# Kernel optimization log

Hardware: AMD Instinct MI355X
Metric: run time of the kernel (lower is better)

## Reference

```python
import jax, jax.numpy as jnp
import numpy as np

N = 100000   # nodes
E = 1600000  # edges
F = 128      # feature / hidden dim
G = 512      # graphs in batch
L = 3        # conv layers
EPS = 1e-5   # batchnorm eps


def _gcn_conv(h, W, b, src, dst, dinv):
    # GCNConv: out = D^{-1/2} (A + I) D^{-1/2} (h W) + b
    hw = h @ W                                   # [N, F]
    norm = dinv[src] * dinv[dst]                 # [E]
    agg = jax.ops.segment_sum(hw[src] * norm[:, None], dst, num_segments=N)
    agg = agg + hw * (dinv * dinv)[:, None]      # self-loop contribution
    return agg + b


def _batchnorm(h, gamma, beta):
    # training-mode BN: batch statistics over the node dimension
    mu = h.mean(axis=0)
    var = h.var(axis=0)
    return gamma * (h - mu) * jax.lax.rsqrt(var + EPS) + beta


def setup_inputs() -> dict:
    key = jax.random.key(0)
    ks = jax.random.split(key, 8)
    x = jax.random.normal(ks[0], (N, F), dtype=jnp.float32)
    edge_index = jax.random.randint(ks[1], (2, E), 0, N)
    batch = jnp.sort(jax.random.randint(ks[2], (N,), 0, G))
    Ws = jax.random.normal(ks[3], (L, F, F), dtype=jnp.float32) / np.float32(np.sqrt(F))
    bs = jnp.zeros((L, F), jnp.float32)
    gammas = jnp.ones((L, F), jnp.float32)
    betas = jnp.zeros((L, F), jnp.float32)
    H = 64  # max(hidden//2, 16)
    w1 = jax.random.normal(ks[4], (2 * F, H), dtype=jnp.float32) / np.float32(np.sqrt(2 * F))
    b1 = jnp.zeros((H,), jnp.float32)
    w2 = jax.random.normal(ks[5], (H, 1), dtype=jnp.float32) / np.float32(np.sqrt(H))
    b2 = jnp.zeros((1,), jnp.float32)
    return dict(x=x, edge_index=edge_index, batch=batch, Ws=Ws, bs=bs,
                gammas=gammas, betas=betas, w1=w1, b1=b1, w2=w2, b2=b2)


def reference(x, edge_index, batch, Ws, bs, gammas, betas, w1, b1, w2, b2):
    src, dst = edge_index[0], edge_index[1]
    # symmetric gcn_norm degrees (self-loops included)
    deg = jax.ops.segment_sum(jnp.ones((E,), x.dtype), dst, num_segments=N) + 1.0
    dinv = jax.lax.rsqrt(deg)
    h = x
    for i in range(L):
        h = _gcn_conv(h, Ws[i], bs[i], src, dst, dinv)
        h = _batchnorm(h, gammas[i], betas[i])
        h = jax.nn.relu(h)  # dropout inactive (eval)
    counts = jax.ops.segment_sum(jnp.ones((N,), h.dtype), batch, num_segments=G)
    mean_pool = jax.ops.segment_sum(h, batch, num_segments=G) / jnp.maximum(counts, 1.0)[:, None]
    max_pool = jax.ops.segment_max(h, batch, num_segments=G)
    max_pool = jnp.where(jnp.isfinite(max_pool), max_pool, 0.0)  # empty segments -> 0
    z = jnp.concatenate([mean_pool, max_pool], axis=1)  # [G, 2F]
    z = jax.nn.relu(z @ w1 + b1)
    return z @ w2 + b2  # [G, 1]
```

## Files before the change

kernel.cpp:

```cpp
#include <hip/hip_runtime.h>
#include <hip/hip_fp16.h>


constexpr int F = 128;
constexpr float BN_EPS = 1e-5f;
constexpr int NB1 = 256;
constexpr int NBKT = 256;

typedef _Float16 f16x8 __attribute__((ext_vector_type(8)));
typedef float f32x4 __attribute__((ext_vector_type(4)));

__global__ void hist_k(const int* __restrict__ dst, int* __restrict__ degi, int E) {
  int stride = gridDim.x * blockDim.x;
  for (int e = blockIdx.x * blockDim.x + threadIdx.x; e < E; e += stride)
    atomicAdd(&degi[dst[e]], 1);
}

__global__ __launch_bounds__(256) void scanA_k(const int* __restrict__ degi, int* __restrict__ bsums,
                                               float* __restrict__ dinv, int n) {
  __shared__ int red[256];
  int tid = threadIdx.x;
  int base = blockIdx.x * 1024 + tid * 4;
  int4 v = *(const int4*)(degi + base);
  if (base + 0 < n) dinv[base + 0] = rsqrtf((float)v.x + 1.0f);
  if (base + 1 < n) dinv[base + 1] = rsqrtf((float)v.y + 1.0f);
  if (base + 2 < n) dinv[base + 2] = rsqrtf((float)v.z + 1.0f);
  if (base + 3 < n) dinv[base + 3] = rsqrtf((float)v.w + 1.0f);
  red[tid] = v.x + v.y + v.z + v.w;
  __syncthreads();
  for (int off = 128; off > 0; off >>= 1) {
    if (tid < off) red[tid] += red[tid + off];
    __syncthreads();
  }
  if (tid == 0) bsums[blockIdx.x] = red[0];
}

__global__ void scanB_k(int* __restrict__ bsums, int nb, int* __restrict__ rowptr, int N) {
  __shared__ int sh[1024];
  int tid = threadIdx.x;
  for (int i = tid; i < nb; i += blockDim.x) sh[i] = bsums[i];
  __syncthreads();
  if (tid == 0) {
    int run = 0;
    for (int i = 0; i < nb; ++i) { int t = sh[i]; sh[i] = run; run += t; }
    rowptr[N] = run;
  }
  __syncthreads();
  for (int i = tid; i < nb; i += blockDim.x) bsums[i] = sh[i];
}

__global__ __launch_bounds__(256) void scanC_k(const int* __restrict__ degi, const int* __restrict__ bsums,
                                               int* __restrict__ rowptr, int n) {
  __shared__ int ts[256];
  int tid = threadIdx.x;
  int base = blockIdx.x * 1024 + tid * 4;
  int4 v = *(const int4*)(degi + base);
  int e0 = v.x, e1 = v.y, e2 = v.z, e3 = v.w;
  int tot = e0 + e1 + e2 + e3;
  ts[tid] = tot;
  __syncthreads();
  for (int off = 1; off < 256; off <<= 1) {
    int add = (tid >= off) ? ts[tid - off] : 0;
    __syncthreads();
    ts[tid] += add;
    __syncthreads();
  }
  int excl = ts[tid] - tot + bsums[blockIdx.x];
  int p0 = excl, p1 = p0 + e0, p2 = p1 + e1, p3 = p2 + e2;
  if (base + 0 < n) rowptr[base + 0] = p0;
  if (base + 1 < n) rowptr[base + 1] = p1;
  if (base + 2 < n) rowptr[base + 2] = p2;
  if (base + 3 < n) rowptr[base + 3] = p3;
}

__global__ __launch_bounds__(256) void part1_k(const int* __restrict__ dst, int* __restrict__ hist, int E) {
  __shared__ int cnt[NBKT];
  int tid = threadIdx.x;
  cnt[tid] = 0;
  __syncthreads();
  int chunk = (E + NB1 - 1) / NB1;
  int s = blockIdx.x * chunk, e = min(s + chunk, E);
  for (int i = s + tid; i < e; i += 256) atomicAdd(&cnt[dst[i] >> 9], 1);
  __syncthreads();
  hist[blockIdx.x * NBKT + tid] = cnt[tid];
}

__global__ __launch_bounds__(1024) void part_scan_k(const int* __restrict__ hist, int* __restrict__ base) {
  __shared__ int sh[1024];
  const int t = threadIdx.x;
  const int per = (NBKT * NB1) / 1024;
  int sum = 0;
  for (int j = 0; j < per; ++j) {
    int i = t * per + j;
    sum += hist[(i & (NB1 - 1)) * NBKT + (i >> 8)];
  }
  sh[t] = sum;
  __syncthreads();
  for (int off = 1; off < 1024; off <<= 1) {
    int v = (t >= off) ? sh[t - off] : 0;
    __syncthreads();
    sh[t] += v;
    __syncthreads();
  }
  int run = sh[t] - sum;
  for (int j = 0; j < per; ++j) {
    int i = t * per + j;
    int v = hist[(i & (NB1 - 1)) * NBKT + (i >> 8)];
    base[i] = run;
    run += v;
  }
}

__global__ __launch_bounds__(256) void part2_k(const int* __restrict__ src, const int* __restrict__ dst,
                                               const int* __restrict__ base, int2* __restrict__ pairbuf, int E) {
  __shared__ int cnt[NBKT];
  __shared__ int baseL[NBKT];
  int tid = threadIdx.x;
  cnt[tid] = 0;
  baseL[tid] = base[tid * NB1 + blockIdx.x];
  __syncthreads();
  int chunk = (E + NB1 - 1) / NB1;
  int s = blockIdx.x * chunk, e = min(s + chunk, E);
  for (int i = s + tid; i < e; i += 256) {
    int sv = src[i], dv = dst[i];
    int b = dv >> 9;
    int r = atomicAdd(&cnt[b], 1);
    pairbuf[baseL[b] + r] = make_int2(sv, dv);
  }
}

__global__ __launch_bounds__(256) void scat2_k(const int2* __restrict__ pairbuf, const int* __restrict__ base,
                                               const int* __restrict__ rowptr, int* __restrict__ cols,
                                               int N, int E) {
  __shared__ int curL[512];
  const int b = blockIdx.x;
  const int tid = threadIdx.x;
  const int n0 = b << 9;
  for (int i = tid; i < 512; i += 256) {
    int node = n0 + i;
    curL[i] = (node < N) ? rowptr[node] : 0;
  }
  __syncthreads();
  int lo = base[b * NB1];
  int hi = (b == NBKT - 1) ? E : base[(b + 1) * NB1];
  for (int t = lo + tid; t < hi; t += 256) {
    int2 pr = pairbuf[t];
    int pos = atomicAdd(&curL[pr.y - n0], 1);
    cols[pos] = pr.x;
  }
}

__global__ __launch_bounds__(128) void wprep_k(const float* __restrict__ W, __half* __restrict__ Wt) {
  const int b = blockIdx.x;
  const int k = threadIdx.x;
  const int l = b >> 7, c = b & 127;
  Wt[(size_t)b * 128 + k] = __float2half(W[(size_t)l * 16384 + k * 128 + c]);
}

__global__ void bnprep_k(const float* __restrict__ stats, const float* __restrict__ gamma,
                         const float* __restrict__ beta, float* __restrict__ scsh,
                         int first, float inv_n) {
  int c = threadIdx.x;
  if (first) { scsh[c] = 1.f; scsh[128 + c] = 0.f; return; }
  float mu = stats[c] * inv_n;
  float var = stats[128 + c] * inv_n - mu * mu;
  float sc = gamma[c] * rsqrtf(var + BN_EPS);
  scsh[c] = sc;
  scsh[128 + c] = beta[c] - mu * sc;
}

__global__ __launch_bounds__(256) void gemm_mfma_k(
    const float* __restrict__ A, const __half* __restrict__ Wt,
    __half* __restrict__ Ch, const float* __restrict__ scsh,
    const float* __restrict__ dinv, int n, int dorelu) {
  __shared__ char Al[64 * 256];
  const int tid = threadIdx.x;
  const int r0 = blockIdx.x * 64;

  {
    const int row = tid & 63;
    const int cb = tid >> 6;
    const int r = r0 + row;
    const int c0 = cb * 32;
    float4 va[8];
    if (r < n) {
      const float* ap = A + (size_t)r * F + c0;
#pragma unroll
      for (int j = 0; j < 8; ++j) va[j] = *(const float4*)(ap + j * 4);
    } else {
#pragma unroll
      for (int j = 0; j < 8; ++j) va[j] = make_float4(0.f, 0.f, 0.f, 0.f);
    }
    union { __half2 h2[16]; int4 q[4]; } u;
#pragma unroll
    for (int j = 0; j < 8; ++j) {
      float4 sc = *(const float4*)(scsh + c0 + j * 4);
      float4 sh = *(const float4*)(scsh + 128 + c0 + j * 4);
      float x0 = fmaf(va[j].x, sc.x, sh.x);
      float x1 = fmaf(va[j].y, sc.y, sh.y);
      float x2 = fmaf(va[j].z, sc.z, sh.z);
      float x3 = fmaf(va[j].w, sc.w, sh.w);
      if (dorelu) {
        x0 = fmaxf(x0, 0.f); x1 = fmaxf(x1, 0.f);
        x2 = fmaxf(x2, 0.f); x3 = fmaxf(x3, 0.f);
      }
      u.h2[2 * j]     = __floats2half2_rn(x0, x1);
      u.h2[2 * j + 1] = __floats2half2_rn(x2, x3);
    }
    const int rowb = row * 256;
    const int swz = (row & 7) << 4;
#pragma unroll
    for (int j = 0; j < 4; ++j) {
      int off = (rowb + cb * 64 + j * 16) ^ swz;
      *(int4*)(Al + off) = u.q[j];
    }
  }
  __syncthreads();

  const int w = tid >> 6, l = tid & 63;
  const int arow = w * 16 + (l & 15);
  const int kg = l >> 4;
  f16x8 af[4];
  {
    const int swz = (arow & 7) << 4;
    const int base = arow * 256 + kg * 16;
#pragma unroll
    for (int kc = 0; kc < 4; ++kc)
      af[kc] = *(const f16x8*)(Al + ((base + kc * 64) ^ swz));
  }
  const int orow = r0 + w * 16 + kg * 4;
  float4 dvv = *(const float4*)(dinv + orow);
  float dvr[4] = {dvv.x, dvv.y, dvv.z, dvv.w};

#pragma unroll
  for (int t = 0; t < 8; ++t) {
    const __half* wp = Wt + ((size_t)(t * 16 + (l & 15)) * 128 + kg * 8);
    f32x4 acc = {0.f, 0.f, 0.f, 0.f};
#pragma unroll
    for (int kc = 0; kc < 4; ++kc) {
      f16x8 bf = *(const f16x8*)(wp + kc * 32);
      acc = __builtin_amdgcn_mfma_f32_16x16x32_f16(af[kc], bf, acc, 0, 0, 0);
    }
    const int ccol = t * 16 + (l & 15);
#pragma unroll
    for (int rr = 0; rr < 4; ++rr) {
      int r = orow + rr;
      if (r < n) Ch[(size_t)r * F + ccol] = __float2half(acc[rr] * dvr[rr]);
    }
  }
}

__global__ __launch_bounds__(256) void spmm_k(const __half* __restrict__ hw, const int* __restrict__ rowptr,
                                              const int* __restrict__ cols, const float* __restrict__ dinv,
                                              const float* __restrict__ bias, float* __restrict__ out, int n) {
  int wid = (blockIdx.x * 256 + threadIdx.x) >> 6;
  int lane = threadIdx.x & 63;
  if (wid >= n) return;
  const __half2* hw2 = (const __half2*)hw;
  float2 vf = __half22float2(hw2[(size_t)wid * 64 + lane]);
  float ax = vf.x, ay = vf.y;
  int j = rowptr[wid];
  const int e = rowptr[wid + 1];
  for (; j + 8 <= e; j += 8) {
    int c0 = cols[j + 0], c1 = cols[j + 1], c2 = cols[j + 2], c3 = cols[j + 3];
    int c4 = cols[j + 4], c5 = cols[j + 5], c6 = cols[j + 6], c7 = cols[j + 7];
    float2 v0 = __half22float2(hw2[(size_t)c0 * 64 + lane]);
    float2 v1 = __half22float2(hw2[(size_t)c1 * 64 + lane]);
    float2 v2 = __half22float2(hw2[(size_t)c2 * 64 + lane]);
    float2 v3 = __half22float2(hw2[(size_t)c3 * 64 + lane]);
    float2 v4 = __half22float2(hw2[(size_t)c4 * 64 + lane]);
    float2 v5 = __half22float2(hw2[(size_t)c5 * 64 + lane]);
    float2 v6 = __half22float2(hw2[(size_t)c6 * 64 + lane]);
    float2 v7 = __half22float2(hw2[(size_t)c7 * 64 + lane]);
    ax += ((v0.x + v1.x) + (v2.x + v3.x)) + ((v4.x + v5.x) + (v6.x + v7.x));
    ay += ((v0.y + v1.y) + (v2.y + v3.y)) + ((v4.y + v5.y) + (v6.y + v7.y));
  }
  if (j + 4 <= e) {
    int c0 = cols[j + 0], c1 = cols[j + 1], c2 = cols[j + 2], c3 = cols[j + 3];
    float2 v0 = __half22float2(hw2[(size_t)c0 * 64 + lane]);
    float2 v1 = __half22float2(hw2[(size_t)c1 * 64 + lane]);
    float2 v2 = __half22float2(hw2[(size_t)c2 * 64 + lane]);
    float2 v3 = __half22float2(hw2[(size_t)c3 * 64 + lane]);
    ax += (v0.x + v1.x) + (v2.x + v3.x);
    ay += (v0.y + v1.y) + (v2.y + v3.y);
    j += 4;
  }
  for (; j < e; ++j) {
    float2 vv = __half22float2(hw2[(size_t)cols[j] * 64 + lane]);
    ax += vv.x;
    ay += vv.y;
  }
  float di = dinv[wid];
  float2 b = ((const float2*)bias)[lane];
  float2 o;
  o.x = fmaf(di, ax, b.x);
  o.y = fmaf(di, ay, b.y);
  ((float2*)out)[(size_t)wid * 64 + lane] = o;
}

__global__ __launch_bounds__(256) void stats_k(const float* __restrict__ h, float* __restrict__ stats, int n) {
  __shared__ float s1[256], s2[256];
  int tid = threadIdx.x;
  int c = tid & 127, half = tid >> 7;
  float a = 0.f, b = 0.f;
  for (int r = blockIdx.x * 2 + half; r < n; r += gridDim.x * 2) {
    float v = h[(size_t)r * F + c];
    a += v;
    b += v * v;
  }
  s1[tid] = a; s2[tid] = b;
  __syncthreads();
  if (tid < 128) {
    atomicAdd(&stats[c], s1[tid] + s1[tid + 128]);
    atomicAdd(&stats[F + c], s2[tid] + s2[tid + 128]);
  }
}

__global__ __launch_bounds__(256) void pool_mlp_k(
    const float* __restrict__ h, const int* __restrict__ batch,
    const float* __restrict__ stats, const float* __restrict__ gamma,
    const float* __restrict__ beta, const float* __restrict__ w1,
    const float* __restrict__ b1, const float* __restrict__ w2,
    const float* __restrict__ b2, float* __restrict__ out,
    int n, float inv_n) {
  __shared__ float psum[4][128];
  __shared__ float pmax[4][128];
  __shared__ float zsh[256];
  __shared__ float part[4][64];
  const int g = blockIdx.x;
  const int tid = threadIdx.x;
  const int wave = tid >> 6, lane = tid & 63;

  int lo = 0, hi = n;
  while (lo < hi) { int m = (lo + hi) >> 1; if (batch[m] < g) lo = m + 1; else hi = m; }
  const int s = lo;
  hi = n;
  while (lo < hi) { int m = (lo + hi) >> 1; if (batch[m] < g + 1) lo = m + 1; else hi = m; }
  const int e = lo;

  const int c = lane * 2;
  float2 st = *(const float2*)(stats + c);
  float2 sq = *(const float2*)(stats + F + c);
  float2 ga = *(const float2*)(gamma + c);
  float2 be = *(const float2*)(beta + c);
  float mu0 = st.x * inv_n, mu1 = st.y * inv_n;
  float sc0 = ga.x * rsqrtf(sq.x * inv_n - mu0 * mu0 + BN_EPS);
  float sc1 = ga.y * rsqrtf(sq.y * inv_n - mu1 * mu1 + BN_EPS);
  float sh0 = be.x - mu0 * sc0;
  float sh1 = be.y - mu1 * sc1;

  float sum0 = 0.f, sum1 = 0.f, mx0 = 0.f, mx1 = 0.f;
#pragma unroll 2
  for (int r = s + wave; r < e; r += 4) {
    float2 v = *(const float2*)(h + (size_t)r * F + c);
    float h0 = fmaxf(fmaf(v.x, sc0, sh0), 0.f);
    float h1 = fmaxf(fmaf(v.y, sc1, sh1), 0.f);
    sum0 += h0; sum1 += h1;
    mx0 = fmaxf(mx0, h0); mx1 = fmaxf(mx1, h1);
  }
  psum[wave][c] = sum0; psum[wave][c + 1] = sum1;
  pmax[wave][c] = mx0;  pmax[wave][c + 1] = mx1;
  __syncthreads();

  if (tid < 128) {
    float sm = psum[0][tid] + psum[1][tid] + psum[2][tid] + psum[3][tid];
    float mx = fmaxf(fmaxf(pmax[0][tid], pmax[1][tid]), fmaxf(pmax[2][tid], pmax[3][tid]));
    float ic = (e > s) ? 1.0f / (float)(e - s) : 0.f;
    zsh[tid] = sm * ic;
    zsh[128 + tid] = mx;
  }
  __syncthreads();

  {
    const int j = lane, q = wave;
    float acc = 0.f;
    const float* wq = w1 + (size_t)q * 64 * 64 + j;
#pragma unroll 8
    for (int i = 0; i < 64; ++i) acc = fmaf(zsh[q * 64 + i], wq[(size_t)i * 64], acc);
    part[q][j] = acc;
  }
  __syncthreads();

  if (tid < 64) {
    float hid = part[0][tid] + part[1][tid] + part[2][tid] + part[3][tid] + b1[tid];
    hid = fmaxf(hid, 0.f) * w2[tid];
    for (int off = 32; off > 0; off >>= 1) hid += __shfl_down(hid, off);
    if (tid == 0) out[g] = hid + b2[0];
  }
}

extern "C" void kernel_launch(void* const* d_in, const int* in_sizes, int n_in,
                              void* d_out, int out_size, void* d_ws, size_t ws_size,
                              hipStream_t stream) {
  const float* x      = (const float*)d_in[0];
  const int*   ei     = (const int*)d_in[1];
  const int*   batch  = (const int*)d_in[2];
  const float* Ws     = (const float*)d_in[3];
  const float* bsv    = (const float*)d_in[4];
  const float* gammas = (const float*)d_in[5];
  const float* betas  = (const float*)d_in[6];
  const float* w1     = (const float*)d_in[7];
  const float* b1     = (const float*)d_in[8];
  const float* w2     = (const float*)d_in[9];
  const float* b2     = (const float*)d_in[10];
  float* out = (float*)d_out;

  const int N = in_sizes[0] / F;
  const int E = in_sizes[1] / 2;
  const int G = out_size;
  const int L = in_sizes[3] / (F * F);
  const int* srcp = ei;
  const int* dstp = ei + E;
  const int NB = (N + 1023) / 1024;

  char* p = (char*)d_ws;
  auto carve = [&](size_t bytes) {
    char* r = p;
    p += (bytes + 255) & ~(size_t)255;
    return r;
  };
  int*    degi    = (int*)carve((size_t)NB * 1024 * 4);
  float*  dinv    = (float*)carve((size_t)N * 4);
  int*    rowptr  = (int*)carve(((size_t)N + 1) * 4);
  int*    colsb   = (int*)carve((size_t)E * 4);
  int*    bsums   = (int*)carve(4096);
  int*    hist    = (int*)carve((size_t)NB1 * NBKT * 4);
  int*    pbase   = (int*)carve((size_t)NB1 * NBKT * 4);
  int2*   pairbuf = (int2*)carve((size_t)E * 8);
  float*  bnstats = (float*)carve(2 * F * 4);
  float*  scsh    = (float*)carve(2 * F * 4);
  __half* wth     = (__half*)carve((size_t)L * F * F * 2);
  __half* hwh     = (__half*)carve((size_t)N * F * 2);
  float*  bufA    = (float*)carve((size_t)N * F * 4);
  (void)ws_size; (void)n_in;

  hipMemsetAsync(degi, 0, (size_t)NB * 1024 * 4, stream);
  hist_k<<<2048, 256, 0, stream>>>(dstp, degi, E);
  scanA_k<<<NB, 256, 0, stream>>>(degi, bsums, dinv, N);
  scanB_k<<<1, 1024, 0, stream>>>(bsums, NB, rowptr, N);
  scanC_k<<<NB, 256, 0, stream>>>(degi, bsums, rowptr, N);
  part1_k<<<NB1, 256, 0, stream>>>(dstp, hist, E);
  part_scan_k<<<1, 1024, 0, stream>>>(hist, pbase);
  part2_k<<<NB1, 256, 0, stream>>>(srcp, dstp, pbase, pairbuf, E);
  scat2_k<<<NBKT, 256, 0, stream>>>(pairbuf, pbase, rowptr, colsb, N, E);
  wprep_k<<<L * F, 128, 0, stream>>>(Ws, wth);

  const float invN = 1.0f / (float)N;
  const int gblocks = (N + 63) / 64;
  for (int l = 0; l < L; ++l) {
    const float* hin = (l == 0) ? x : bufA;
    const float* ga  = (l == 0) ? gammas : gammas + (size_t)(l - 1) * F;
    const float* be  = (l == 0) ? betas : betas + (size_t)(l - 1) * F;
    bnprep_k<<<1, 128, 0, stream>>>(bnstats, ga, be, scsh, (l == 0) ? 1 : 0, invN);
    gemm_mfma_k<<<gblocks, 256, 0, stream>>>(hin, wth + (size_t)l * F * F, hwh, scsh, dinv, N,
                                             (l == 0) ? 0 : 1);
    hipMemsetAsync(bnstats, 0, 2 * F * 4, stream);
    spmm_k<<<(N * 64 + 255) / 256, 256, 0, stream>>>(hwh, rowptr, colsb, dinv,
                                                     bsv + (size_t)l * F, bufA, N);
    stats_k<<<512, 256, 0, stream>>>(bufA, bnstats, N);
  }

  pool_mlp_k<<<G, 256, 0, stream>>>(bufA, batch, bnstats, gammas + (size_t)(L - 1) * F,
                                    betas + (size_t)(L - 1) * F, w1, b1, w2, b2, out, N, invN);
}
```

Before: 699.6 us.

## Fuse BN stats into SpMM, store aggregates in fp16, derive degrees in scatter

Drops the separate degree histogram and three-pass scan. Each bucket in the scatter kernel now counts its own node degrees, computes rowptr and dinv locally, and then scatters. The SpMM becomes a persistent grid-stride kernel that writes the aggregate as fp16 and accumulates the BatchNorm sum and sum of squares, which removes the stats kernel and its full fp32 reread. The GEMM and pooling kernels read the fp16 aggregate, halving intermediate traffic at some cost in precision.

```diff
diff --git a/kernel.cpp b/kernel.cpp
--- a/kernel.cpp
+++ b/kernel.cpp
@@ -9,69 +9,6 @@
 
 typedef _Float16 f16x8 __attribute__((ext_vector_type(8)));
 typedef float f32x4 __attribute__((ext_vector_type(4)));
-
-__global__ void hist_k(const int* __restrict__ dst, int* __restrict__ degi, int E) {
-  int stride = gridDim.x * blockDim.x;
-  for (int e = blockIdx.x * blockDim.x + threadIdx.x; e < E; e += stride)
-    atomicAdd(&degi[dst[e]], 1);
-}
-
-__global__ __launch_bounds__(256) void scanA_k(const int* __restrict__ degi, int* __restrict__ bsums,
-                                               float* __restrict__ dinv, int n) {
-  __shared__ int red[256];
-  int tid = threadIdx.x;
-  int base = blockIdx.x * 1024 + tid * 4;
-  int4 v = *(const int4*)(degi + base);
-  if (base + 0 < n) dinv[base + 0] = rsqrtf((float)v.x + 1.0f);
-  if (base + 1 < n) dinv[base + 1] = rsqrtf((float)v.y + 1.0f);
-  if (base + 2 < n) dinv[base + 2] = rsqrtf((float)v.z + 1.0f);
-  if (base + 3 < n) dinv[base + 3] = rsqrtf((float)v.w + 1.0f);
-  red[tid] = v.x + v.y + v.z + v.w;
-  __syncthreads();
-  for (int off = 128; off > 0; off >>= 1) {
-    if (tid < off) red[tid] += red[tid + off];
-    __syncthreads();
-  }
-  if (tid == 0) bsums[blockIdx.x] = red[0];
-}
-
-__global__ void scanB_k(int* __restrict__ bsums, int nb, int* __restrict__ rowptr, int N) {
-  __shared__ int sh[1024];
-  int tid = threadIdx.x;
-  for (int i = tid; i < nb; i += blockDim.x) sh[i] = bsums[i];
-  __syncthreads();
-  if (tid == 0) {
-    int run = 0;
-    for (int i = 0; i < nb; ++i) { int t = sh[i]; sh[i] = run; run += t; }
-    rowptr[N] = run;
-  }
-  __syncthreads();
-  for (int i = tid; i < nb; i += blockDim.x) bsums[i] = sh[i];
-}
-
-__global__ __launch_bounds__(256) void scanC_k(const int* __restrict__ degi, const int* __restrict__ bsums,
-                                               int* __restrict__ rowptr, int n) {
-  __shared__ int ts[256];
-  int tid = threadIdx.x;
-  int base = blockIdx.x * 1024 + tid * 4;
-  int4 v = *(const int4*)(degi + base);
-  int e0 = v.x, e1 = v.y, e2 = v.z, e3 = v.w;
-  int tot = e0 + e1 + e2 + e3;
-  ts[tid] = tot;
-  __syncthreads();
-  for (int off = 1; off < 256; off <<= 1) {
-    int add = (tid >= off) ? ts[tid - off] : 0;
-    __syncthreads();
-    ts[tid] += add;
-    __syncthreads();
-  }
-  int excl = ts[tid] - tot + bsums[blockIdx.x];
-  int p0 = excl, p1 = p0 + e0, p2 = p1 + e1, p3 = p2 + e2;
-  if (base + 0 < n) rowptr[base + 0] = p0;
-  if (base + 1 < n) rowptr[base + 1] = p1;
-  if (base + 2 < n) rowptr[base + 2] = p2;
-  if (base + 3 < n) rowptr[base + 3] = p3;
-}
 
 __global__ __launch_bounds__(256) void part1_k(const int* __restrict__ dst, int* __restrict__ hist, int E) {
   __shared__ int cnt[NBKT];
@@ -130,22 +67,42 @@
 }
 
 __global__ __launch_bounds__(256) void scat2_k(const int2* __restrict__ pairbuf, const int* __restrict__ base,
-                                               const int* __restrict__ rowptr, int* __restrict__ cols,
-                                               int N, int E) {
-  __shared__ int curL[512];
+                                               int* __restrict__ rowptr, int* __restrict__ cols,
+                                               float* __restrict__ dinv, int N, int E) {
+  __shared__ int cnt[512];
+  __shared__ int cur[512];
+  __shared__ int ssum[256];
   const int b = blockIdx.x;
   const int tid = threadIdx.x;
   const int n0 = b << 9;
-  for (int i = tid; i < 512; i += 256) {
-    int node = n0 + i;
-    curL[i] = (node < N) ? rowptr[node] : 0;
-  }
-  __syncthreads();
-  int lo = base[b * NB1];
-  int hi = (b == NBKT - 1) ? E : base[(b + 1) * NB1];
+  cnt[tid] = 0; cnt[tid + 256] = 0;
+  __syncthreads();
+  const int lo = base[b * NB1];
+  const int hi = (b == NBKT - 1) ? E : base[(b + 1) * NB1];
+  for (int t = lo + tid; t < hi; t += 256)
+    atomicAdd(&cnt[pairbuf[t].y - n0], 1);
+  __syncthreads();
+  const int c0 = cnt[2 * tid], c1 = cnt[2 * tid + 1];
+  const int s = c0 + c1;
+  ssum[tid] = s;
+  __syncthreads();
+  for (int off = 1; off < 256; off <<= 1) {
+    int v = (tid >= off) ? ssum[tid - off] : 0;
+    __syncthreads();
+    ssum[tid] += v;
+    __syncthreads();
+  }
+  const int excl = ssum[tid] - s;
+  const int p0 = lo + excl, p1 = p0 + c0;
+  const int node0 = n0 + 2 * tid, node1 = node0 + 1;
+  if (node0 < N) { rowptr[node0] = p0; dinv[node0] = rsqrtf((float)c0 + 1.f); }
+  if (node1 < N) { rowptr[node1] = p1; dinv[node1] = rsqrtf((float)c1 + 1.f); }
+  cur[2 * tid] = p0; cur[2 * tid + 1] = p1;
+  if (b == NBKT - 1 && tid == 255) rowptr[N] = E;
+  __syncthreads();
   for (int t = lo + tid; t < hi; t += 256) {
     int2 pr = pairbuf[t];
-    int pos = atomicAdd(&curL[pr.y - n0], 1);
+    int pos = atomicAdd(&cur[pr.y - n0], 1);
     cols[pos] = pr.x;
   }
 }
@@ -170,9 +127,9 @@
 }
 
 __global__ __launch_bounds__(256) void gemm_mfma_k(
-    const float* __restrict__ A, const __half* __restrict__ Wt,
-    __half* __restrict__ Ch, const float* __restrict__ scsh,
-    const float* __restrict__ dinv, int n, int dorelu) {
+    const float* __restrict__ Af, const __half* __restrict__ Ah,
+    const __half* __restrict__ Wt, __half* __restrict__ Ch,
+    const float* __restrict__ scsh, const float* __restrict__ dinv, int n, int dorelu) {
   __shared__ char Al[64 * 256];
   const int tid = threadIdx.x;
   const int r0 = blockIdx.x * 64;
@@ -182,30 +139,47 @@
     const int cb = tid >> 6;
     const int r = r0 + row;
     const int c0 = cb * 32;
-    float4 va[8];
-    if (r < n) {
-      const float* ap = A + (size_t)r * F + c0;
-#pragma unroll
-      for (int j = 0; j < 8; ++j) va[j] = *(const float4*)(ap + j * 4);
+    float xv[32];
+    if (Af) {
+      if (r < n) {
+        const float* ap = Af + (size_t)r * F + c0;
+#pragma unroll
+        for (int j = 0; j < 8; ++j) {
+          float4 v = *(const float4*)(ap + j * 4);
+          xv[4 * j] = v.x; xv[4 * j + 1] = v.y; xv[4 * j + 2] = v.z; xv[4 * j + 3] = v.w;
+        }
+      } else {
+#pragma unroll
+        for (int j = 0; j < 32; ++j) xv[j] = 0.f;
+      }
     } else {
-#pragma unroll
-      for (int j = 0; j < 8; ++j) va[j] = make_float4(0.f, 0.f, 0.f, 0.f);
+      if (r < n) {
+        const int4* ap = (const int4*)(Ah + (size_t)r * F + c0);
+#pragma unroll
+        for (int j = 0; j < 4; ++j) {
+          union { int4 q; __half2 h2[4]; } u;
+          u.q = ap[j];
+#pragma unroll
+          for (int p = 0; p < 4; ++p) {
+            float2 f = __half22float2(u.h2[p]);
+            xv[8 * j + 2 * p] = f.x;
+            xv[8 * j + 2 * p + 1] = f.y;
+          }
+        }
+      } else {
+#pragma unroll
+        for (int j = 0; j < 32; ++j) xv[j] = 0.f;
+      }
     }
     union { __half2 h2[16]; int4 q[4]; } u;
 #pragma unroll
-    for (int j = 0; j < 8; ++j) {
-      float4 sc = *(const float4*)(scsh + c0 + j * 4);
-      float4 sh = *(const float4*)(scsh + 128 + c0 + j * 4);
-      float x0 = fmaf(va[j].x, sc.x, sh.x);
-      float x1 = fmaf(va[j].y, sc.y, sh.y);
-      float x2 = fmaf(va[j].z, sc.z, sh.z);
-      float x3 = fmaf(va[j].w, sc.w, sh.w);
-      if (dorelu) {
-        x0 = fmaxf(x0, 0.f); x1 = fmaxf(x1, 0.f);
-        x2 = fmaxf(x2, 0.f); x3 = fmaxf(x3, 0.f);
-      }
-      u.h2[2 * j]     = __floats2half2_rn(x0, x1);
-      u.h2[2 * j + 1] = __floats2half2_rn(x2, x3);
+    for (int p = 0; p < 16; ++p) {
+      float2 sc = *(const float2*)(scsh + c0 + 2 * p);
+      float2 sh = *(const float2*)(scsh + 128 + c0 + 2 * p);
+      float x0 = fmaf(xv[2 * p], sc.x, sh.x);
+      float x1 = fmaf(xv[2 * p + 1], sc.y, sh.y);
+      if (dorelu) { x0 = fmaxf(x0, 0.f); x1 = fmaxf(x1, 0.f); }
+      u.h2[p] = __floats2half2_rn(x0, x1);
     }
     const int rowb = row * 256;
     const int swz = (row & 7) << 4;
@@ -252,72 +226,74 @@
 
 __global__ __launch_bounds__(256) void spmm_k(const __half* __restrict__ hw, const int* __restrict__ rowptr,
                                               const int* __restrict__ cols, const float* __restrict__ dinv,
-                                              const float* __restrict__ bias, float* __restrict__ out, int n) {
-  int wid = (blockIdx.x * 256 + threadIdx.x) >> 6;
-  int lane = threadIdx.x & 63;
-  if (wid >= n) return;
+                                              const float* __restrict__ bias, __half* __restrict__ outh,
+                                              float* __restrict__ stats, int n) {
+  const int lane = threadIdx.x & 63;
+  const int wv = (blockIdx.x << 2) | (threadIdx.x >> 6);
+  const int stride = gridDim.x << 2;
   const __half2* hw2 = (const __half2*)hw;
-  float2 vf = __half22float2(hw2[(size_t)wid * 64 + lane]);
-  float ax = vf.x, ay = vf.y;
-  int j = rowptr[wid];
-  const int e = rowptr[wid + 1];
-  for (; j + 8 <= e; j += 8) {
-    int c0 = cols[j + 0], c1 = cols[j + 1], c2 = cols[j + 2], c3 = cols[j + 3];
-    int c4 = cols[j + 4], c5 = cols[j + 5], c6 = cols[j + 6], c7 = cols[j + 7];
-    float2 v0 = __half22float2(hw2[(size_t)c0 * 64 + lane]);
-    float2 v1 = __half22float2(hw2[(size_t)c1 * 64 + lane]);
-    float2 v2 = __half22float2(hw2[(size_t)c2 * 64 + lane]);
-    float2 v3 = __half22float2(hw2[(size_t)c3 * 64 + lane]);
-    float2 v4 = __half22float2(hw2[(size_t)c4 * 64 + lane]);
-    float2 v5 = __half22float2(hw2[(size_t)c5 * 64 + lane]);
-    float2 v6 = __half22float2(hw2[(size_t)c6 * 64 + lane]);
-    float2 v7 = __half22float2(hw2[(size_t)c7 * 64 + lane]);
-    ax += ((v0.x + v1.x) + (v2.x + v3.x)) + ((v4.x + v5.x) + (v6.x + v7.x));
-    ay += ((v0.y + v1.y) + (v2.y + v3.y)) + ((v4.y + v5.y) + (v6.y + v7.y));
-  }
-  if (j + 4 <= e) {
-    int c0 = cols[j + 0], c1 = cols[j + 1], c2 = cols[j + 2], c3 = cols[j + 3];
-    float2 v0 = __half22float2(hw2[(size_t)c0 * 64 + lane]);
-    float2 v1 = __half22float2(hw2[(size_t)c1 * 64 + lane]);
-    float2 v2 = __half22float2(hw2[(size_t)c2 * 64 + lane]);
-    float2 v3 = __half22float2(hw2[(size_t)c3 * 64 + lane]);
-    ax += (v0.x + v1.x) + (v2.x + v3.x);
-    ay += (v0.y + v1.y) + (v2.y + v3.y);
-    j += 4;
-  }
-  for (; j < e; ++j) {
-    float2 vv = __half22float2(hw2[(size_t)cols[j] * 64 + lane]);
-    ax += vv.x;
-    ay += vv.y;
-  }
-  float di = dinv[wid];
-  float2 b = ((const float2*)bias)[lane];
-  float2 o;
-  o.x = fmaf(di, ax, b.x);
-  o.y = fmaf(di, ay, b.y);
-  ((float2*)out)[(size_t)wid * 64 + lane] = o;
-}
-
-__global__ __launch_bounds__(256) void stats_k(const float* __restrict__ h, float* __restrict__ stats, int n) {
-  __shared__ float s1[256], s2[256];
-  int tid = threadIdx.x;
-  int c = tid & 127, half = tid >> 7;
-  float a = 0.f, b = 0.f;
-  for (int r = blockIdx.x * 2 + half; r < n; r += gridDim.x * 2) {
-    float v = h[(size_t)r * F + c];
-    a += v;
-    b += v * v;
-  }
-  s1[tid] = a; s2[tid] = b;
-  __syncthreads();
-  if (tid < 128) {
-    atomicAdd(&stats[c], s1[tid] + s1[tid + 128]);
-    atomicAdd(&stats[F + c], s2[tid] + s2[tid + 128]);
+  const float2 b = ((const float2*)bias)[lane];
+  float s0 = 0.f, s1 = 0.f, q0 = 0.f, q1 = 0.f;
+
+  for (int wid = wv; wid < n; wid += stride) {
+    float2 vf = __half22float2(hw2[(size_t)wid * 64 + lane]);
+    float ax = vf.x, ay = vf.y;
+    int j = rowptr[wid];
+    const int e = rowptr[wid + 1];
+    for (; j + 8 <= e; j += 8) {
+      int c0 = cols[j + 0], c1 = cols[j + 1], c2 = cols[j + 2], c3 = cols[j + 3];
+      int c4 = cols[j + 4], c5 = cols[j + 5], c6 = cols[j + 6], c7 = cols[j + 7];
+      float2 v0 = __half22float2(hw2[(size_t)c0 * 64 + lane]);
+      float2 v1 = __half22float2(hw2[(size_t)c1 * 64 + lane]);
+      float2 v2 = __half22float2(hw2[(size_t)c2 * 64 + lane]);
+      float2 v3 = __half22float2(hw2[(size_t)c3 * 64 + lane]);
+      float2 v4 = __half22float2(hw2[(size_t)c4 * 64 + lane]);
+      float2 v5 = __half22float2(hw2[(size_t)c5 * 64 + lane]);
+      float2 v6 = __half22float2(hw2[(size_t)c6 * 64 + lane]);
+      float2 v7 = __half22float2(hw2[(size_t)c7 * 64 + lane]);
+      ax += ((v0.x + v1.x) + (v2.x + v3.x)) + ((v4.x + v5.x) + (v6.x + v7.x));
+      ay += ((v0.y + v1.y) + (v2.y + v3.y)) + ((v4.y + v5.y) + (v6.y + v7.y));
+    }
+    if (j + 4 <= e) {
+      int c0 = cols[j + 0], c1 = cols[j + 1], c2 = cols[j + 2], c3 = cols[j + 3];
+      float2 v0 = __half22float2(hw2[(size_t)c0 * 64 + lane]);
+      float2 v1 = __half22float2(hw2[(size_t)c1 * 64 + lane]);
+      float2 v2 = __half22float2(hw2[(size_t)c2 * 64 + lane]);
+      float2 v3 = __half22float2(hw2[(size_t)c3 * 64 + lane]);
+      ax += (v0.x + v1.x) + (v2.x + v3.x);
+      ay += (v0.y + v1.y) + (v2.y + v3.y);
+      j += 4;
+    }
+    for (; j < e; ++j) {
+      float2 vv = __half22float2(hw2[(size_t)cols[j] * 64 + lane]);
+      ax += vv.x;
+      ay += vv.y;
+    }
+    float di = dinv[wid];
+    __half2 oh = __floats2half2_rn(fmaf(di, ax, b.x), fmaf(di, ay, b.y));
+    ((__half2*)outh)[(size_t)wid * 64 + lane] = oh;
+    float2 of = __half22float2(oh);
+    s0 += of.x; s1 += of.y;
+    q0 += of.x * of.x; q1 += of.y * of.y;
+  }
+
+  __shared__ float rs0[256], rs1[256], rq0[256], rq1[256];
+  rs0[threadIdx.x] = s0; rs1[threadIdx.x] = s1;
+  rq0[threadIdx.x] = q0; rq1[threadIdx.x] = q1;
+  __syncthreads();
+  if (threadIdx.x < 64) {
+    const int l = threadIdx.x;
+    atomicAdd(&stats[2 * l], rs0[l] + rs0[l + 64] + rs0[l + 128] + rs0[l + 192]);
+    atomicAdd(&stats[F + 2 * l], rq0[l] + rq0[l + 64] + rq0[l + 128] + rq0[l + 192]);
+  } else if (threadIdx.x < 128) {
+    const int l = threadIdx.x - 64;
+    atomicAdd(&stats[2 * l + 1], rs1[l] + rs1[l + 64] + rs1[l + 128] + rs1[l + 192]);
+    atomicAdd(&stats[F + 2 * l + 1], rq1[l] + rq1[l + 64] + rq1[l + 128] + rq1[l + 192]);
   }
 }
 
 __global__ __launch_bounds__(256) void pool_mlp_k(
-    const float* __restrict__ h, const int* __restrict__ batch,
+    const __half* __restrict__ h, const int* __restrict__ batch,
     const float* __restrict__ stats, const float* __restrict__ gamma,
     const float* __restrict__ beta, const float* __restrict__ w1,
     const float* __restrict__ b1, const float* __restrict__ w2,
@@ -349,10 +325,11 @@
   float sh0 = be.x - mu0 * sc0;
   float sh1 = be.y - mu1 * sc1;
 
+  const __half2* h2 = (const __half2*)h;
   float sum0 = 0.f, sum1 = 0.f, mx0 = 0.f, mx1 = 0.f;
 #pragma unroll 2
   for (int r = s + wave; r < e; r += 4) {
-    float2 v = *(const float2*)(h + (size_t)r * F + c);
+    float2 v = __half22float2(h2[(size_t)r * 64 + lane]);
     float h0 = fmaxf(fmaf(v.x, sc0, sh0), 0.f);
     float h1 = fmaxf(fmaf(v.y, sc1, sh1), 0.f);
     sum0 += h0; sum1 += h1;
@@ -411,7 +388,6 @@
   const int L = in_sizes[3] / (F * F);
   const int* srcp = ei;
   const int* dstp = ei + E;
-  const int NB = (N + 1023) / 1024;
 
   char* p = (char*)d_ws;
   auto carve = [&](size_t bytes) {
@@ -419,11 +395,9 @@
     p += (bytes + 255) & ~(size_t)255;
     return r;
   };
-  int*    degi    = (int*)carve((size_t)NB * 1024 * 4);
   float*  dinv    = (float*)carve((size_t)N * 4);
   int*    rowptr  = (int*)carve(((size_t)N + 1) * 4);
   int*    colsb   = (int*)carve((size_t)E * 4);
-  int*    bsums   = (int*)carve(4096);
   int*    hist    = (int*)carve((size_t)NB1 * NBKT * 4);
   int*    pbase   = (int*)carve((size_t)NB1 * NBKT * 4);
   int2*   pairbuf = (int2*)carve((size_t)E * 8);
@@ -431,35 +405,29 @@
   float*  scsh    = (float*)carve(2 * F * 4);
   __half* wth     = (__half*)carve((size_t)L * F * F * 2);
   __half* hwh     = (__half*)carve((size_t)N * F * 2);
-  float*  bufA    = (float*)carve((size_t)N * F * 4);
+  __half* aggh    = (__half*)carve((size_t)N * F * 2);
   (void)ws_size; (void)n_in;
 
-  hipMemsetAsync(degi, 0, (size_t)NB * 1024 * 4, stream);
-  hist_k<<<2048, 256, 0, stream>>>(dstp, degi, E);
-  scanA_k<<<NB, 256, 0, stream>>>(degi, bsums, dinv, N);
-  scanB_k<<<1, 1024, 0, stream>>>(bsums, NB, rowptr, N);
-  scanC_k<<<NB, 256, 0, stream>>>(degi, bsums, rowptr, N);
   part1_k<<<NB1, 256, 0, stream>>>(dstp, hist, E);
   part_scan_k<<<1, 1024, 0, stream>>>(hist, pbase);
   part2_k<<<NB1, 256, 0, stream>>>(srcp, dstp, pbase, pairbuf, E);
-  scat2_k<<<NBKT, 256, 0, stream>>>(pairbuf, pbase, rowptr, colsb, N, E);
+  scat2_k<<<NBKT, 256, 0, stream>>>(pairbuf, pbase, rowptr, colsb, dinv, N, E);
   wprep_k<<<L * F, 128, 0, stream>>>(Ws, wth);
 
   const float invN = 1.0f / (float)N;
   const int gblocks = (N + 63) / 64;
   for (int l = 0; l < L; ++l) {
-    const float* hin = (l == 0) ? x : bufA;
-    const float* ga  = (l == 0) ? gammas : gammas + (size_t)(l - 1) * F;
-    const float* be  = (l == 0) ? betas : betas + (size_t)(l - 1) * F;
+    const float* ga = (l == 0) ? gammas : gammas + (size_t)(l - 1) * F;
+    const float* be = (l == 0) ? betas : betas + (size_t)(l - 1) * F;
     bnprep_k<<<1, 128, 0, stream>>>(bnstats, ga, be, scsh, (l == 0) ? 1 : 0, invN);
-    gemm_mfma_k<<<gblocks, 256, 0, stream>>>(hin, wth + (size_t)l * F * F, hwh, scsh, dinv, N,
+    gemm_mfma_k<<<gblocks, 256, 0, stream>>>((l == 0) ? x : nullptr, (l == 0) ? nullptr : aggh,
+                                             wth + (size_t)l * F * F, hwh, scsh, dinv, N,
                                              (l == 0) ? 0 : 1);
     hipMemsetAsync(bnstats, 0, 2 * F * 4, stream);
-    spmm_k<<<(N * 64 + 255) / 256, 256, 0, stream>>>(hwh, rowptr, colsb, dinv,
-                                                     bsv + (size_t)l * F, bufA, N);
-    stats_k<<<512, 256, 0, stream>>>(bufA, bnstats, N);
-  }
-
-  pool_mlp_k<<<G, 256, 0, stream>>>(bufA, batch, bnstats, gammas + (size_t)(L - 1) * F,
+    spmm_k<<<1536, 256, 0, stream>>>(hwh, rowptr, colsb, dinv, bsv + (size_t)l * F,
+                                     aggh, bnstats, N);
+  }
+
+  pool_mlp_k<<<G, 256, 0, stream>>>(aggh, batch, bnstats, gammas + (size_t)(L - 1) * F,
                                     betas + (size_t)(L - 1) * F, w1, b1, w2, b2, out, N, invN);
 }
```

Result: slower. 718.4 us (+2.7%).
